# Performance work log

Measured on AMD Instinct MI355X. Metric: run time of the kernel, lower is better.

The kernel has to match this reference:

```python
import jax, jax.numpy as jnp
import numpy as np

WD, WH, WW = 7, 7, 7  # 3D window size


def _relative_position_index():
    # Matches the torch buffer construction exactly.
    coords = np.stack(np.meshgrid(np.arange(WD), np.arange(WH), np.arange(WW), indexing='ij'))  # [3,wd,wh,ww]
    cf = coords.reshape(3, -1)                      # [3, n]
    rel = cf[:, :, None] - cf[:, None, :]           # [3, n, n]
    rel = rel.transpose(1, 2, 0).copy()             # [n, n, 3]
    rel[..., 0] += WD - 1
    rel[..., 1] += WH - 1
    rel[..., 2] += WW - 1
    rel[..., 0] *= (2 * WH - 1) * (2 * WW - 1)
    rel[..., 1] *= (2 * WW - 1)
    return rel.sum(-1).astype(np.int32)             # [n, n] in [0, 2197)


def setup_inputs() -> dict:
    key = jax.random.key(0)
    ks = jax.random.split(key, 10)
    DIM, H = 192, 6
    B, N, NW = 256, WD * WH * WW, 64  # b = batch*num_windows, NW divides B
    TABLE = (2 * WD - 1) * (2 * WH - 1) * (2 * WW - 1)  # 2197
    w_std = 0.02
    mask = jnp.where(jax.random.uniform(ks[2], (NW, N, N)) < 0.1, -100.0, 0.0).astype(jnp.float32)
    return {
        'x_q': jax.random.normal(ks[0], (B, N, DIM), jnp.float32),
        'x_kv': jax.random.normal(ks[1], (B, N, DIM), jnp.float32),
        'mask': mask,
        'q_w': jax.random.normal(ks[3], (DIM, DIM), jnp.float32) * w_std,
        'q_b': jnp.zeros((DIM,), jnp.float32),
        'kv_w': jax.random.normal(ks[4], (2 * DIM, DIM), jnp.float32) * w_std,
        'kv_b': jnp.zeros((2 * DIM,), jnp.float32),
        'proj_w': jax.random.normal(ks[5], (DIM, DIM), jnp.float32) * w_std,
        'proj_b': jnp.zeros((DIM,), jnp.float32),
        'rpb_table': jax.random.normal(ks[6], (TABLE, H), jnp.float32) * w_std,
        'rpi': jnp.asarray(_relative_position_index()),
    }


def reference(x_q, x_kv, mask, q_w, q_b, kv_w, kv_b, proj_w, proj_b, rpb_table, rpi):
    b, n, c = x_q.shape
    h = rpb_table.shape[-1]
    d = c // h
    scale = d ** (-0.5)
    # projections (torch Linear: y = x @ W.T + b)
    q = (x_q @ q_w.T + q_b).reshape(b, n, h, d)
    kv = x_kv @ kv_w.T + kv_b                      # [b, n, 2c]
    k = kv[..., :c].reshape(b, n, h, d)
    v = kv[..., c:].reshape(b, n, h, d)
    # windowed QK^T
    attn = jnp.einsum('bnhd,bmhd->bhnm', q * scale, k)  # [b, h, n, n]
    # gathered relative-position bias
    rpb = rpb_table[rpi[:n, :n].reshape(-1)].reshape(n, n, h).transpose(2, 0, 1)  # [h, n, n]
    attn = attn + rpb[None]
    # window mask add
    nw = mask.shape[0]
    attn = attn.reshape(b // nw, nw, h, n, n) + mask[None, :, None]
    attn = jax.nn.softmax(attn.reshape(b, h, n, n), axis=-1)
    out = jnp.einsum('bhnm,bmhd->bnhd', attn, v).reshape(b, n, c)
    return out @ proj_w.T + proj_b
```

## Files before the change

kernel.cpp:

```cpp
#include <hip/hip_runtime.h>
#include <hip/hip_bf16.h>
#include <cstdint>

#define B_    256
#define N_    343
#define C_    192
#define H_    6
#define D_    32
#define NW_   64
#define M_    (B_*N_)
#define NN_   (N_*N_)
#define VTS_  352
#define VLS_  360
#define RPG_  86
#define SCALE_ 0.17677669529663687f
#define LOG2E_ 1.4426950408889634f
#define SCALE_LOG2E_ (SCALE_ * LOG2E_)

typedef unsigned short ushort_t;
typedef __attribute__((ext_vector_type(8))) short short8;
typedef __attribute__((ext_vector_type(4))) float f32x4;
typedef __attribute__((ext_vector_type(16))) float f32x16;

__device__ __forceinline__ float b2f(unsigned int u) {
    return __uint_as_float(u << 16);
}
__device__ __forceinline__ unsigned int f2b(float f) {
    unsigned int x = __float_as_uint(f);
    x += 0x7FFFu + ((x >> 16) & 1u);
    return x >> 16;
}
__device__ __forceinline__ unsigned int cvt_pk(float a, float b) {
    unsigned int r;
    asm("v_cvt_pk_bf16_f32 %0, %1, %2" : "=v"(r) : "v"(a), "v"(b));
    return r;
}
__device__ __forceinline__ void pswap(unsigned int &x, unsigned int &y) {
    asm("v_permlane32_swap_b32 %0, %1" : "+v"(x), "+v"(y));
}

__global__ __launch_bounds__(256) void wcvt(
    const float* __restrict__ qw, const float* __restrict__ kvw,
    const float* __restrict__ pw, ushort_t* __restrict__ wb)
{
    int i = blockIdx.x * 256 + threadIdx.x;
    if (i >= 36864) return;
    float4 v;
    if (i < 9216)       v = ((const float4*)qw)[i];
    else if (i < 27648) v = ((const float4*)kvw)[i - 9216];
    else                v = ((const float4*)pw)[i - 27648];
    uint2 u;
    u.x = cvt_pk(v.x, v.y);
    u.y = cvt_pk(v.z, v.w);
    ((uint2*)wb)[i] = u;
}

__global__ __launch_bounds__(512, 2) void gemm_qkv(
    const float* __restrict__ xq, const float* __restrict__ xkv,
    const ushort_t* __restrict__ wb,
    const float* __restrict__ qbias, const float* __restrict__ kvbias,
    ushort_t* __restrict__ qx, ushort_t* __restrict__ kx,
    ushort_t* __restrict__ vtb)
{
    __shared__ ushort_t wls[192 * 200];
    __shared__ ushort_t xls[128 * 200];

    const int t = threadIdx.x, wv = t >> 6, lane = t & 63;
    const int quad = lane >> 4, col = lane & 15;
    const int lid = blockIdx.x;
    const int xcd = lid & 7, idx = lid >> 3;
    const int wg = (xcd < 2 ? xcd * 258 : 2 * 258 + (xcd - 2) * 257) + idx;
    const int jsel = wg % 3;
    const int m0 = (wg / 3) * 128;
    const ushort_t* W = wb + (size_t)jsel * 36864;
    const float* Xf = (jsel == 0) ? xq : xkv;
    const float* bias = (jsel == 0) ? qbias : (jsel == 1 ? kvbias : kvbias + 192);
    const float alpha = (jsel == 0) ? SCALE_LOG2E_ : 1.0f;

    const float* xsrc = Xf + (size_t)m0 * 192;

    float4 xa[6];
    #pragma unroll
    for (int i = 0; i < 6; ++i)
        xa[i] = *(const float4*)(xsrc + (size_t)(i * 512 + t) * 4);

    for (int c = t; c < 4608; c += 512) {
        int row = c / 24, off = (c % 24) * 8;
        *(short8*)(wls + row * 200 + off) = *(const short8*)(W + row * 192 + off);
    }

    #pragma unroll
    for (int i = 0; i < 6; ++i) {
        int c = i * 512 + t;
        int row = c / 48, off = (c % 48) * 4;
        uint2 u; u.x = cvt_pk(xa[i].x, xa[i].y); u.y = cvt_pk(xa[i].z, xa[i].w);
        *(uint2*)(xls + row * 200 + off) = u;
    }
    float4 xb[6];
    #pragma unroll
    for (int i = 0; i < 6; ++i)
        xb[i] = *(const float4*)(xsrc + (size_t)(3072 + i * 512 + t) * 4);
    #pragma unroll
    for (int i = 0; i < 6; ++i) {
        int c = 3072 + i * 512 + t;
        int row = c / 48, off = (c % 48) * 4;
        uint2 u; u.x = cvt_pk(xb[i].x, xb[i].y); u.y = cvt_pk(xb[i].z, xb[i].w);
        *(uint2*)(xls + row * 200 + off) = u;
    }
    __syncthreads();

    short8 xf[6];
    {
        const ushort_t* xlp = xls + (wv * 16 + col) * 200;
        #pragma unroll
        for (int kt = 0; kt < 6; ++kt)
            xf[kt] = *(const short8*)(xlp + kt * 32 + quad * 8);
    }

    f32x4 acc[12] = {};
    #pragma unroll
    for (int kt = 0; kt < 6; ++kt)
        #pragma unroll
        for (int ct = 0; ct < 12; ++ct) {
            short8 wf = *(const short8*)(wls + (ct * 16 + col) * 200 + kt * 32 + quad * 8);
            acc[ct] = __builtin_amdgcn_mfma_f32_16x16x32_bf16(wf, xf[kt], acc[ct], 0, 0, 0);
        }

    if (jsel < 2) {
        ushort_t* o16 = (jsel == 0) ? qx : kx;
        int m = m0 + wv * 16 + col;
        int bb = m / N_, nn = m - bb * N_;
        #pragma unroll
        for (int ct = 0; ct < 12; ++ct) {
            float4 bv = *(const float4*)(bias + ct * 16 + quad * 4);
            int hh = ct >> 1;
            int dbase = (ct & 1) * 16 + quad * 4;
            float v0 = (acc[ct][0] + bv.x) * alpha;
            float v1 = (acc[ct][1] + bv.y) * alpha;
            float v2 = (acc[ct][2] + bv.z) * alpha;
            float v3 = (acc[ct][3] + bv.w) * alpha;
            uint2 pk;
            pk.x = cvt_pk(v0, v1);
            pk.y = cvt_pk(v2, v3);
            *(uint2*)(o16 + (((size_t)bb * H_ + hh) * N_ + nn) * D_ + dbase) = pk;
        }
    } else {
        int m = m0 + wv * 16 + col;
        int bb = m / N_, nn = m - bb * N_;
        #pragma unroll
        for (int ct = 0; ct < 12; ++ct) {
            float4 bv = *(const float4*)(bias + ct * 16 + quad * 4);
            int hh = ct >> 1;
            int d0 = (ct & 1) * 16 + quad * 4;
            unsigned int u01 = cvt_pk(acc[ct][0] + bv.x, acc[ct][1] + bv.y);
            unsigned int u23 = cvt_pk(acc[ct][2] + bv.z, acc[ct][3] + bv.w);
            ushort_t* vp = vtb + (((size_t)bb * H_ + hh) * D_ + d0) * VTS_ + nn;
            vp[0]            = (ushort_t)u01;
            vp[VTS_]         = (ushort_t)(u01 >> 16);
            vp[2 * VTS_]     = (ushort_t)u23;
            vp[3 * VTS_]     = (ushort_t)(u23 >> 16);
        }
    }
}

__global__ __launch_bounds__(512, 4) void gemm_out(
    const ushort_t* __restrict__ aob, const ushort_t* __restrict__ wb,
    const float* __restrict__ pbias, float* __restrict__ out)
{
    __shared__ ushort_t wls[192 * 200];

    const int t = threadIdx.x, wv = t >> 6, lane = t & 63;
    const int quad = lane >> 4, col = lane & 15;
    const int m0 = blockIdx.x * 128;
    const ushort_t* W = wb + (size_t)3 * 36864;

    short8 xf[6];
    {
        const ushort_t* xp = aob + (size_t)(m0 + wv * 16 + col) * 192;
        #pragma unroll
        for (int kt = 0; kt < 6; ++kt)
            xf[kt] = *(const short8*)(xp + kt * 32 + quad * 8);
    }
    for (int c = t; c < 4608; c += 512) {
        int row = c / 24, off = (c % 24) * 8;
        *(short8*)(wls + row * 200 + off) = *(const short8*)(W + row * 192 + off);
    }
    __syncthreads();

    f32x4 acc[12] = {};
    #pragma unroll
    for (int kt = 0; kt < 6; ++kt)
        #pragma unroll
        for (int ct = 0; ct < 12; ++ct) {
            short8 wf = *(const short8*)(wls + (ct * 16 + col) * 200 + kt * 32 + quad * 8);
            acc[ct] = __builtin_amdgcn_mfma_f32_16x16x32_bf16(wf, xf[kt], acc[ct], 0, 0, 0);
        }

    int m = m0 + wv * 16 + col;
    #pragma unroll
    for (int ct = 0; ct < 12; ++ct) {
        float4 bv = *(const float4*)(pbias + ct * 16 + quad * 4);
        float4 vo;
        vo.x = acc[ct][0] + bv.x; vo.y = acc[ct][1] + bv.y;
        vo.z = acc[ct][2] + bv.z; vo.w = acc[ct][3] + bv.w;
        *(float4*)(out + (size_t)m * 192 + ct * 16 + quad * 4) = vo;
    }
}

__global__ __launch_bounds__(256) void rpb_gather_b(
    const float* __restrict__ table, const int* __restrict__ rpi,
    ushort_t* __restrict__ rpbt)
{
    int n = blockIdx.x;
    for (int m = threadIdx.x; m < N_; m += 256) {
        int id = rpi[n * N_ + m];
        int mg = m >> 2, mi = m & 3;
        #pragma unroll
        for (int h = 0; h < H_; ++h)
            rpbt[((((size_t)h * RPG_ + mg) * N_) + n) * 4 + mi] =
                (ushort_t)f2b(table[(size_t)id * H_ + h] * LOG2E_);
    }
}

__global__ __launch_bounds__(256) void mask_bits(
    const float* __restrict__ mask, unsigned int* __restrict__ mbt)
{
    int gw   = blockIdx.x * 4 + (threadIdx.x >> 6);
    int lane = threadIdx.x & 63;
    int n = gw % N_, w = gw / N_;
    if (w >= NW_) return;
    const float* mrow = mask + ((size_t)w * N_ + n) * N_;
    #pragma unroll
    for (int seg = 0; seg < 6; ++seg) {
        int m = seg * 64 + lane;
        float v = (m < N_) ? mrow[m] : -100.f;
        unsigned long long bm = __ballot(v > -50.f);
        if (lane < 2)
            mbt[((size_t)w * 12 + seg * 2 + lane) * N_ + n] =
                (unsigned int)(bm >> (lane * 32));
    }
}

__global__ __launch_bounds__(256) void vt_pad(ushort_t* __restrict__ vtb)
{
    int bh = blockIdx.x;
    for (int i = threadIdx.x; i < D_ * (VTS_ - N_); i += 256) {
        int d = i / (VTS_ - N_), m = N_ + i % (VTS_ - N_);
        vtb[((size_t)bh * D_ + d) * VTS_ + m] = 0;
    }
}

__global__ __launch_bounds__(256, 3) void attn_mfma(
    const ushort_t* __restrict__ qb, const ushort_t* __restrict__ kb,
    const ushort_t* __restrict__ vtb, const ushort_t* __restrict__ rpbt,
    const unsigned int* __restrict__ mbt, ushort_t* __restrict__ aob)
{
    __shared__ ushort_t ks[352 * 40];
    __shared__ ushort_t vls[32 * VLS_];

    const int t = threadIdx.x, wv = t >> 6, lane = t & 63;
    const int hh = lane >> 5, c = lane & 31;
    const int lid = blockIdx.x;
    const int wg = (lid & 7) * 576 + (lid >> 3);
    const int qt = wg % 3;
    const int bhx = wg / 3;
    const int h = bhx % H_, b = bhx / H_;
    const int bh = b * H_ + h;
    const int w  = b & (NW_ - 1);
    const int n0 = qt * 128 + wv * 32;

    const ushort_t* kbase = kb + (size_t)bh * (N_ * D_);
    for (int cc = t; cc < (N_ * D_) / 8; cc += 256) {
        int row = cc >> 2, off = (cc & 3) * 8;
        *(short8*)(ks + row * 40 + off) = *(const short8*)(kbase + cc * 8);
    }
    const ushort_t* vbase = vtb + (size_t)bh * (D_ * VTS_);
    for (int cc = t; cc < (D_ * VTS_) / 8; cc += 256) {
        int row = cc / 44, off = (cc % 44) * 8;
        *(short8*)(vls + row * VLS_ + off) = *(const short8*)(vbase + cc * 8);
    }

    int nn = n0 + c; if (nn > N_ - 1) nn = N_ - 1;
    const ushort_t* qp = qb + ((size_t)bh * N_ + nn) * D_;
    short8 qf0 = *(const short8*)(qp + hh * 8);
    short8 qf1 = *(const short8*)(qp + 16 + hh * 8);

    unsigned int dwv[12];
    {
        const unsigned int* mbp = mbt + (size_t)w * 12 * N_ + nn;
        #pragma unroll
        for (int i = 0; i < 12; ++i) dwv[i] = mbp[i * N_];
    }
    const uint2* rp2 = (const uint2*)rpbt + (size_t)h * (RPG_ * N_) + nn;

    __syncthreads();

    f32x16 oacc = {};
    float sum = 0.f;

    #pragma unroll
    for (int kt = 0; kt < 11; ++kt) {
        const ushort_t* krow = ks + (kt * 32 + c) * 40 + hh * 8;
        short8 ka  = *(const short8*)(krow);
        short8 kb2 = *(const short8*)(krow + 16);
        f32x16 s = {};
        s = __builtin_amdgcn_mfma_f32_32x32x16_bf16(ka,  qf0, s, 0, 0, 0);
        s = __builtin_amdgcn_mfma_f32_32x32x16_bf16(kb2, qf1, s, 0, 0, 0);

        unsigned int nibs = dwv[kt] >> (hh * 4);
        unsigned int pk[8];
        #pragma unroll
        for (int g = 0; g < 4; ++g) {
            int mg = kt * 8 + 2 * g + hh;
            if (mg > RPG_ - 1) mg = RPG_ - 1;
            uint2 rv = rp2[(size_t)mg * N_];
            unsigned int nib = (nibs >> (g * 8)) & 0xFu;
            float e0 = __builtin_exp2f(s[4*g+0] + b2f(rv.x & 0xffffu));
            float e1 = __builtin_exp2f(s[4*g+1] + b2f(rv.x >> 16));
            float e2 = __builtin_exp2f(s[4*g+2] + b2f(rv.y & 0xffffu));
            float e3 = __builtin_exp2f(s[4*g+3] + b2f(rv.y >> 16));
            e0 = (nib & 1u) ? e0 : 0.f;
            e1 = (nib & 2u) ? e1 : 0.f;
            e2 = (nib & 4u) ? e2 : 0.f;
            e3 = (nib & 8u) ? e3 : 0.f;
            sum += (e0 + e1) + (e2 + e3);
            pk[2*g]   = cvt_pk(e0, e1);
            pk[2*g+1] = cvt_pk(e2, e3);
        }
        pswap(pk[0], pk[2]);
        pswap(pk[1], pk[3]);
        pswap(pk[4], pk[6]);
        pswap(pk[5], pk[7]);
        union { short8 s8; unsigned int u[4]; } pf1, pf2;
        pf1.u[0] = pk[0]; pf1.u[1] = pk[1]; pf1.u[2] = pk[2]; pf1.u[3] = pk[3];
        pf2.u[0] = pk[4]; pf2.u[1] = pk[5]; pf2.u[2] = pk[6]; pf2.u[3] = pk[7];

        const ushort_t* vrow = vls + c * VLS_ + kt * 32 + hh * 8;
        short8 vf1 = *(const short8*)(vrow);
        short8 vf2 = *(const short8*)(vrow + 16);
        oacc = __builtin_amdgcn_mfma_f32_32x32x16_bf16(vf1, pf1.s8, oacc, 0, 0, 0);
        oacc = __builtin_amdgcn_mfma_f32_32x32x16_bf16(vf2, pf2.s8, oacc, 0, 0, 0);
    }

    sum += __shfl_xor(sum, 32);

    int n = n0 + c;
    if (n < N_) {
        float inv = 1.0f / sum;
        ushort_t* op = aob + ((size_t)b * N_ + n) * C_ + h * D_ + hh * 4;
        #pragma unroll
        for (int g = 0; g < 4; ++g) {
            uint2 pkk;
            pkk.x = cvt_pk(oacc[4*g+0] * inv, oacc[4*g+1] * inv);
            pkk.y = cvt_pk(oacc[4*g+2] * inv, oacc[4*g+3] * inv);
            *(uint2*)(op + g * 8) = pkk;
        }
    }
}

extern "C" void kernel_launch(void* const* d_in, const int* in_sizes, int n_in,
                              void* d_out, int out_size, void* d_ws, size_t ws_size,
                              hipStream_t stream)
{
    const float* x_q    = (const float*)d_in[0];
    const float* x_kv   = (const float*)d_in[1];
    const float* mask   = (const float*)d_in[2];
    const float* q_w    = (const float*)d_in[3];
    const float* q_b    = (const float*)d_in[4];
    const float* kv_w   = (const float*)d_in[5];
    const float* kv_b   = (const float*)d_in[6];
    const float* proj_w = (const float*)d_in[7];
    const float* proj_b = (const float*)d_in[8];
    const float* rpb_t  = (const float*)d_in[9];
    const int*   rpi    = (const int*)d_in[10];
    float* out = (float*)d_out;

    const size_t QKV  = (size_t)B_ * H_ * N_ * D_;
    const size_t QKV2 = (size_t)B_ * H_ * D_ * VTS_;
    char* ws = (char*)d_ws;
    ushort_t* qx   = (ushort_t*)ws;
    ushort_t* kx   = qx + QKV;
    ushort_t* vtb  = kx + QKV;
    ushort_t* aob  = vtb + QKV2;
    ushort_t* rpbt = aob + QKV;
    ushort_t* wb   = rpbt + (size_t)H_ * RPG_ * N_ * 4;
    unsigned int* mbt = (unsigned int*)(wb + 147456);

    wcvt<<<144, 256, 0, stream>>>(q_w, kv_w, proj_w, wb);
    rpb_gather_b<<<N_, 256, 0, stream>>>(rpb_t, rpi, rpbt);
    mask_bits<<<(NW_ * N_) / 4, 256, 0, stream>>>(mask, mbt);
    vt_pad<<<B_ * H_, 256, 0, stream>>>(vtb);
    gemm_qkv<<<2058, 512, 0, stream>>>(
        x_q, x_kv, wb, q_b, kv_b, qx, kx, vtb);
    attn_mfma<<<4608, 256, 0, stream>>>(qx, kx, vtb, rpbt, mbt, aob);
    gemm_out<<<M_/128, 512, 0, stream>>>(aob, wb, proj_b, out);
}
```

Before: 383.0 us.

## Make QKV GEMM persistent over four tiles with register-prefetched X loads

```diff
diff --git a/kernel.cpp b/kernel.cpp
--- a/kernel.cpp
+++ b/kernel.cpp
@@ -64,31 +64,37 @@
 {
     __shared__ ushort_t wls[192 * 200];
     __shared__ ushort_t xls[128 * 200];
+    __shared__ float    bls[192];
 
     const int t = threadIdx.x, wv = t >> 6, lane = t & 63;
     const int quad = lane >> 4, col = lane & 15;
     const int lid = blockIdx.x;
     const int xcd = lid & 7, idx = lid >> 3;
-    const int wg = (xcd < 2 ? xcd * 258 : 2 * 258 + (xcd - 2) * 257) + idx;
+    const int wg = (xcd < 4 ? xcd * 65 : 4 * 65 + (xcd - 4) * 64) + idx;
     const int jsel = wg % 3;
-    const int m0 = (wg / 3) * 128;
+    const int g = wg / 3;
     const ushort_t* W = wb + (size_t)jsel * 36864;
     const float* Xf = (jsel == 0) ? xq : xkv;
     const float* bias = (jsel == 0) ? qbias : (jsel == 1 ? kvbias : kvbias + 192);
     const float alpha = (jsel == 0) ? SCALE_LOG2E_ : 1.0f;
 
-    const float* xsrc = Xf + (size_t)m0 * 192;
-
-    float4 xa[6];
-    #pragma unroll
-    for (int i = 0; i < 6; ++i)
-        xa[i] = *(const float4*)(xsrc + (size_t)(i * 512 + t) * 4);
-
     for (int c = t; c < 4608; c += 512) {
         int row = c / 24, off = (c % 24) * 8;
         *(short8*)(wls + row * 200 + off) = *(const short8*)(W + row * 192 + off);
     }
-
+    if (t < 48) ((float4*)bls)[t] = ((const float4*)bias)[t];
+
+    float4 xa[6], xb[6];
+    {
+        int tl = g * 4; if (tl > 685) tl = 685;
+        const float* xsrc = Xf + (size_t)tl * 128 * 192;
+        #pragma unroll
+        for (int i = 0; i < 6; ++i)
+            xa[i] = *(const float4*)(xsrc + (size_t)(i * 512 + t) * 4);
+        #pragma unroll
+        for (int i = 0; i < 6; ++i)
+            xb[i] = *(const float4*)(xsrc + (size_t)(3072 + i * 512 + t) * 4);
+    }
     #pragma unroll
     for (int i = 0; i < 6; ++i) {
         int c = i * 512 + t;
@@ -96,10 +102,6 @@
         uint2 u; u.x = cvt_pk(xa[i].x, xa[i].y); u.y = cvt_pk(xa[i].z, xa[i].w);
         *(uint2*)(xls + row * 200 + off) = u;
     }
-    float4 xb[6];
-    #pragma unroll
-    for (int i = 0; i < 6; ++i)
-        xb[i] = *(const float4*)(xsrc + (size_t)(3072 + i * 512 + t) * 4);
     #pragma unroll
     for (int i = 0; i < 6; ++i) {
         int c = 3072 + i * 512 + t;
@@ -109,56 +111,92 @@
     }
     __syncthreads();
 
-    short8 xf[6];
-    {
-        const ushort_t* xlp = xls + (wv * 16 + col) * 200;
-        #pragma unroll
-        for (int kt = 0; kt < 6; ++kt)
-            xf[kt] = *(const short8*)(xlp + kt * 32 + quad * 8);
-    }
-
-    f32x4 acc[12] = {};
-    #pragma unroll
-    for (int kt = 0; kt < 6; ++kt)
-        #pragma unroll
-        for (int ct = 0; ct < 12; ++ct) {
-            short8 wf = *(const short8*)(wls + (ct * 16 + col) * 200 + kt * 32 + quad * 8);
-            acc[ct] = __builtin_amdgcn_mfma_f32_16x16x32_bf16(wf, xf[kt], acc[ct], 0, 0, 0);
-        }
-
-    if (jsel < 2) {
-        ushort_t* o16 = (jsel == 0) ? qx : kx;
-        int m = m0 + wv * 16 + col;
-        int bb = m / N_, nn = m - bb * N_;
-        #pragma unroll
-        for (int ct = 0; ct < 12; ++ct) {
-            float4 bv = *(const float4*)(bias + ct * 16 + quad * 4);
-            int hh = ct >> 1;
-            int dbase = (ct & 1) * 16 + quad * 4;
-            float v0 = (acc[ct][0] + bv.x) * alpha;
-            float v1 = (acc[ct][1] + bv.y) * alpha;
-            float v2 = (acc[ct][2] + bv.z) * alpha;
-            float v3 = (acc[ct][3] + bv.w) * alpha;
-            uint2 pk;
-            pk.x = cvt_pk(v0, v1);
-            pk.y = cvt_pk(v2, v3);
-            *(uint2*)(o16 + (((size_t)bb * H_ + hh) * N_ + nn) * D_ + dbase) = pk;
-        }
-    } else {
-        int m = m0 + wv * 16 + col;
-        int bb = m / N_, nn = m - bb * N_;
-        #pragma unroll
-        for (int ct = 0; ct < 12; ++ct) {
-            float4 bv = *(const float4*)(bias + ct * 16 + quad * 4);
-            int hh = ct >> 1;
-            int d0 = (ct & 1) * 16 + quad * 4;
-            unsigned int u01 = cvt_pk(acc[ct][0] + bv.x, acc[ct][1] + bv.y);
-            unsigned int u23 = cvt_pk(acc[ct][2] + bv.z, acc[ct][3] + bv.w);
-            ushort_t* vp = vtb + (((size_t)bb * H_ + hh) * D_ + d0) * VTS_ + nn;
-            vp[0]            = (ushort_t)u01;
-            vp[VTS_]         = (ushort_t)(u01 >> 16);
-            vp[2 * VTS_]     = (ushort_t)u23;
-            vp[3 * VTS_]     = (ushort_t)(u23 >> 16);
+    for (int tt = 0; tt < 4; ++tt) {
+        const int tile = g * 4 + tt;
+        const bool valid = tile < 686;
+
+        short8 xf[6];
+        {
+            const ushort_t* xlp = xls + (wv * 16 + col) * 200;
+            #pragma unroll
+            for (int kt = 0; kt < 6; ++kt)
+                xf[kt] = *(const short8*)(xlp + kt * 32 + quad * 8);
+        }
+        if (tt < 3) {
+            int tn = tile + 1; if (tn > 685) tn = 685;
+            const float* xs2 = Xf + (size_t)tn * 128 * 192;
+            #pragma unroll
+            for (int i = 0; i < 6; ++i)
+                xa[i] = *(const float4*)(xs2 + (size_t)(i * 512 + t) * 4);
+            #pragma unroll
+            for (int i = 0; i < 6; ++i)
+                xb[i] = *(const float4*)(xs2 + (size_t)(3072 + i * 512 + t) * 4);
+        }
+        __syncthreads();
+
+        if (valid) {
+            f32x4 acc[12] = {};
+            #pragma unroll
+            for (int kt = 0; kt < 6; ++kt)
+                #pragma unroll
+                for (int ct = 0; ct < 12; ++ct) {
+                    short8 wf = *(const short8*)(wls + (ct * 16 + col) * 200 + kt * 32 + quad * 8);
+                    acc[ct] = __builtin_amdgcn_mfma_f32_16x16x32_bf16(wf, xf[kt], acc[ct], 0, 0, 0);
+                }
+
+            if (jsel < 2) {
+                ushort_t* o16 = (jsel == 0) ? qx : kx;
+                int m = tile * 128 + wv * 16 + col;
+                int bb = m / N_, nn = m - bb * N_;
+                #pragma unroll
+                for (int ct = 0; ct < 12; ++ct) {
+                    float4 bv = *(const float4*)(bls + ct * 16 + quad * 4);
+                    int hh = ct >> 1;
+                    int dbase = (ct & 1) * 16 + quad * 4;
+                    float v0 = (acc[ct][0] + bv.x) * alpha;
+                    float v1 = (acc[ct][1] + bv.y) * alpha;
+                    float v2 = (acc[ct][2] + bv.z) * alpha;
+                    float v3 = (acc[ct][3] + bv.w) * alpha;
+                    uint2 pk;
+                    pk.x = cvt_pk(v0, v1);
+                    pk.y = cvt_pk(v2, v3);
+                    *(uint2*)(o16 + (((size_t)bb * H_ + hh) * N_ + nn) * D_ + dbase) = pk;
+                }
+            } else {
+                int m = tile * 128 + wv * 16 + col;
+                int bb = m / N_, nn = m - bb * N_;
+                #pragma unroll
+                for (int ct = 0; ct < 12; ++ct) {
+                    float4 bv = *(const float4*)(bls + ct * 16 + quad * 4);
+                    int hh = ct >> 1;
+                    int d0 = (ct & 1) * 16 + quad * 4;
+                    unsigned int u01 = cvt_pk(acc[ct][0] + bv.x, acc[ct][1] + bv.y);
+                    unsigned int u23 = cvt_pk(acc[ct][2] + bv.z, acc[ct][3] + bv.w);
+                    ushort_t* vp = vtb + (((size_t)bb * H_ + hh) * D_ + d0) * VTS_ + nn;
+                    vp[0]            = (ushort_t)u01;
+                    vp[VTS_]         = (ushort_t)(u01 >> 16);
+                    vp[2 * VTS_]     = (ushort_t)u23;
+                    vp[3 * VTS_]     = (ushort_t)(u23 >> 16);
+                }
+            }
+        }
+
+        if (tt < 3) {
+            #pragma unroll
+            for (int i = 0; i < 6; ++i) {
+                int c = i * 512 + t;
+                int row = c / 48, off = (c % 48) * 4;
+                uint2 u; u.x = cvt_pk(xa[i].x, xa[i].y); u.y = cvt_pk(xa[i].z, xa[i].w);
+                *(uint2*)(xls + row * 200 + off) = u;
+            }
+            #pragma unroll
+            for (int i = 0; i < 6; ++i) {
+                int c = 3072 + i * 512 + t;
+                int row = c / 48, off = (c % 48) * 4;
+                uint2 u; u.x = cvt_pk(xb[i].x, xb[i].y); u.y = cvt_pk(xb[i].z, xb[i].w);
+                *(uint2*)(xls + row * 200 + off) = u;
+            }
+            __syncthreads();
         }
     }
 }
@@ -390,7 +428,7 @@
     rpb_gather_b<<<N_, 256, 0, stream>>>(rpb_t, rpi, rpbt);
     mask_bits<<<(NW_ * N_) / 4, 256, 0, stream>>>(mask, mbt);
     vt_pad<<<B_ * H_, 256, 0, stream>>>(vtb);
-    gemm_qkv<<<2058, 512, 0, stream>>>(
+    gemm_qkv<<<516, 512, 0, stream>>>(
         x_q, x_kv, wb, q_b, kv_b, qx, kx, vtb);
     attn_mfma<<<4608, 256, 0, stream>>>(qx, kx, vtb, rpbt, mbt, aob);
     gemm_out<<<M_/128, 512, 0, stream>>>(aob, wb, proj_b, out);
```

New measurement: 381.8 us. Within noise of the previous version (-0.3%).
